# Performance work log

Measured on AMD Instinct MI355X. Metric: run time of the kernel, lower is better.

The kernel has to match this reference:

```python
import jax, jax.numpy as jnp
import numpy as np

ALPHA = 0.2  # leaky relu slope
NEG = -9e15


def setup_inputs() -> dict:
    key = jax.random.key(0)
    k1, k2, k3, k4 = jax.random.split(key, 4)
    B, N, Fin, Fout = 16, 2048, 256, 256
    h = jax.random.normal(k1, (B, N, Fin), dtype=jnp.float32)
    adj = jax.random.randint(k2, (B, N, N), 0, 2, dtype=jnp.int32)
    # xavier_uniform with gain 1.414 on [B, Fin, Fout] (fan over last two dims)
    limW = 1.414 * np.sqrt(6.0 / (Fin + Fout))
    W = jax.random.uniform(k3, (B, Fin, Fout), minval=-limW, maxval=limW, dtype=jnp.float32)
    lima = 1.414 * np.sqrt(6.0 / (2 * Fout + 1))
    a = jax.random.uniform(k4, (B, 2 * Fout, 1), minval=-lima, maxval=lima, dtype=jnp.float32)
    return {"h": h, "adj": adj, "W": W, "a": a}


def reference(h, adj, W, a):
    Fout = W.shape[-1]
    Wh = jnp.einsum('bnf,bfo->bno', h, W)                 # [B,N,Fout]
    Wh1 = jnp.einsum('bno,bo->bn', Wh, a[:, :Fout, 0])    # [B,N]
    Wh2 = jnp.einsum('bno,bo->bn', Wh, a[:, Fout:, 0])    # [B,N]
    e = Wh1[:, :, None] + Wh2[:, None, :]                 # [B,N,N]
    e = jnp.where(e > 0, e, ALPHA * e)                    # leaky relu
    att = jnp.where(adj > 0, e, NEG)
    att = jax.nn.softmax(att, axis=1)                     # NOTE: dim=1 as in source
    # dropout: eval mode -> identity
    h_prime = jnp.einsum('bij,bjo->bio', att, Wh)         # [B,N,Fout]
    return jax.nn.elu(h_prime)                            # concat=True
```

## Files before the change

kernel.cpp:

```cpp
#include <hip/hip_runtime.h>
#include <hip/hip_bf16.h>

typedef unsigned short u16;
typedef unsigned long long u64;
typedef __attribute__((ext_vector_type(8))) short bf16x8;
typedef __attribute__((ext_vector_type(4))) float f32x4;

#define NB 16
#define NN 2048
#define FF 256
#define LOG2E 1.4426950408889634f

__device__ __forceinline__ u16 f2bf(float x) {
    union { float f; unsigned u; } v; v.f = x;
    unsigned r = v.u + 0x7fffu + ((v.u >> 16) & 1u);
    return (u16)(r >> 16);
}

#define GLD_LDS(g, l) __builtin_amdgcn_global_load_lds((const __attribute__((address_space(1))) void*)(g), (__attribute__((address_space(3))) void*)(l), 16, 0, 0)

__global__ __launch_bounds__(256) void k_prep_w(const float* __restrict__ W, const float* __restrict__ a,
                                                u16* __restrict__ WT, float* __restrict__ u1, float* __restrict__ u2) {
    int b = blockIdx.y, t = threadIdx.x;
    __shared__ float a1s[FF], a2s[FF];
    a1s[t] = a[b*2*FF + t];
    a2s[t] = a[b*2*FF + FF + t];
    __syncthreads();
    int f = blockIdx.x*64 + (t >> 2);
    int o0 = (t & 3) * 64;
    const float* wrow = W + (size_t)(b*FF + f)*FF + o0;
    u16* wtb = WT + (size_t)b*FF*FF;
    float s1 = 0.f, s2 = 0.f;
#pragma unroll
    for (int c = 0; c < 16; ++c) {
        float4 v = *(const float4*)(wrow + c*4);
        int o = o0 + c*4;
        s1 += v.x*a1s[o] + v.y*a1s[o+1] + v.z*a1s[o+2] + v.w*a1s[o+3];
        s2 += v.x*a2s[o] + v.y*a2s[o+1] + v.z*a2s[o+2] + v.w*a2s[o+3];
        wtb[(size_t)(o+0)*FF + f] = f2bf(v.x);
        wtb[(size_t)(o+1)*FF + f] = f2bf(v.y);
        wtb[(size_t)(o+2)*FF + f] = f2bf(v.z);
        wtb[(size_t)(o+3)*FF + f] = f2bf(v.w);
    }
    s1 += __shfl_xor(s1, 1); s1 += __shfl_xor(s1, 2);
    s2 += __shfl_xor(s2, 1); s2 += __shfl_xor(s2, 2);
    if ((t & 3) == 0) { u1[b*FF + f] = s1; u2[b*FF + f] = s2; }
}

__global__ __launch_bounds__(256) void k_prep_h(const float* __restrict__ h, const float* __restrict__ u1,
                                                const float* __restrict__ u2, u16* __restrict__ hbf,
                                                float* __restrict__ Wh1, float* __restrict__ Wh2) {
    int b = blockIdx.y, t = threadIdx.x;
    __shared__ float u1s[FF], u2s[FF];
    u1s[t] = u1[b*FF + t];
    u2s[t] = u2[b*FF + t];
    __syncthreads();
    int wave = t >> 6, lane = t & 63;
    int i = blockIdx.x*4 + wave;
    size_t rowoff = ((size_t)(b*NN + i))*FF + lane*4;
    float4 v = *(const float4*)(h + rowoff);
    u16 h0 = f2bf(v.x), h1 = f2bf(v.y), h2 = f2bf(v.z), h3 = f2bf(v.w);
    unsigned p0 = (unsigned)h0 | ((unsigned)h1 << 16);
    unsigned p1 = (unsigned)h2 | ((unsigned)h3 << 16);
    uint2 pk; pk.x = p0; pk.y = p1;
    *(uint2*)(hbf + rowoff) = pk;
    int o = lane*4;
    float s1 = v.x*u1s[o] + v.y*u1s[o+1] + v.z*u1s[o+2] + v.w*u1s[o+3];
    float s2 = v.x*u2s[o] + v.y*u2s[o+1] + v.z*u2s[o+2] + v.w*u2s[o+3];
#pragma unroll
    for (int off = 32; off > 0; off >>= 1) { s1 += __shfl_xor(s1, off); s2 += __shfl_xor(s2, off); }
    if (lane == 0) { Wh1[b*NN + i] = s1*LOG2E; Wh2[b*NN + i] = s2*LOG2E; }
}

__global__ __launch_bounds__(256) void k_gemm1(const u16* __restrict__ WT, const u16* __restrict__ hbf,
                                               u16* __restrict__ WhT) {
    int b = blockIdx.z;
    int o0 = blockIdx.y * 64;
    int i0 = blockIdx.x * 256;
    int t = threadIdx.x, lane = t & 63, w = t >> 6;
    __shared__ alignas(16) u16 At[64*64];
    __shared__ alignas(16) u16 Btl[256*64];
    const u16* WTb = WT + (size_t)b*FF*FF;
    const u16* hb  = hbf + (size_t)b*NN*FF;

    f32x4 acc[4][4];
#pragma unroll
    for (int x = 0; x < 4; ++x)
#pragma unroll
        for (int y = 0; y < 4; ++y) acc[x][y] = (f32x4)0.f;

    for (int kk = 0; kk < 4; ++kk) {
        int k0 = kk*64;
#pragma unroll
        for (int is = 0; is < 2; ++is) {
            int s = is*256 + t;
            int row = s >> 3, jbp = s & 7;
            int jbl = jbp ^ (row & 7);
            GLD_LDS(WTb + (size_t)(o0+row)*FF + k0 + jbl*8, &At[s*8]);
        }
#pragma unroll
        for (int is = 0; is < 8; ++is) {
            int s = is*256 + t;
            int row = s >> 3, jbp = s & 7;
            int jbl = jbp ^ (row & 7);
            GLD_LDS(hb + (size_t)(i0+row)*FF + k0 + jbl*8, &Btl[s*8]);
        }
        __syncthreads();
#pragma unroll
        for (int kc = 0; kc < 2; ++kc) {
            int jl = kc*4 + (lane >> 4);
            bf16x8 af[4], bfr[4];
#pragma unroll
            for (int mi = 0; mi < 4; ++mi) {
                int r = mi*16 + (lane & 15);
                af[mi] = *(const bf16x8*)&At[r*64 + (jl ^ (r & 7))*8];
            }
#pragma unroll
            for (int ni = 0; ni < 4; ++ni) {
                int r = w*64 + ni*16 + (lane & 15);
                bfr[ni] = *(const bf16x8*)&Btl[r*64 + (jl ^ (r & 7))*8];
            }
#pragma unroll
            for (int mi = 0; mi < 4; ++mi)
#pragma unroll
                for (int ni = 0; ni < 4; ++ni)
                    acc[mi][ni] = __builtin_amdgcn_mfma_f32_16x16x32_bf16(af[mi], bfr[ni], acc[mi][ni], 0, 0, 0);
        }
        __syncthreads();
    }
    u16* Wo = WhT + (size_t)b*FF*NN;
#pragma unroll
    for (int mi = 0; mi < 4; ++mi)
#pragma unroll
        for (int ni = 0; ni < 4; ++ni) {
            int i = i0 + w*64 + ni*16 + (lane & 15);
#pragma unroll
            for (int rr = 0; rr < 4; ++rr) {
                int o = o0 + mi*16 + (lane >> 4)*4 + rr;
                Wo[(size_t)o*NN + i] = f2bf(acc[mi][ni][rr]);
            }
        }
}

__global__ __launch_bounds__(256) void k_colsum(const int* __restrict__ adj, const float* __restrict__ Wh1,
                                                const float* __restrict__ Wh2, float* __restrict__ pS,
                                                u64* __restrict__ packed) {
    int b = blockIdx.z, ic = blockIdx.y, jt = blockIdx.x;
    int t = threadIdx.x, lane = t & 63, wave = t >> 6;
    __shared__ float wh1s[256];
    int ibase = ic*256;
    wh1s[t] = Wh1[b*NN + ibase + t];
    __syncthreads();
    int j = jt*256 + t;
    float wh2j = Wh2[b*NN + j];
    const int* acol = adj + (size_t)b*NN*NN + (size_t)ibase*NN + j;
    u64* prow = packed + ((size_t)(b*NN + ibase))*32 + jt*4 + wave;
    float s = 0.f;
    for (int ii = 0; ii < 256; ii += 8) {
        int v[8];
#pragma unroll
        for (int r = 0; r < 8; ++r) v[r] = acol[(size_t)(ii + r)*NN];
#pragma unroll
        for (int r = 0; r < 8; ++r) {
            bool p = v[r] > 0;
            u64 m = __ballot(p);
            if (lane == 0) prow[(size_t)(ii + r)*32] = m;
            float tt = wh1s[ii + r] + wh2j;
            float lr = fmaxf(tt, 0.2f*tt);
            float e = exp2f(lr);
            s += p ? e : 0.f;
        }
    }
    pS[((size_t)(b*8 + ic))*NN + j] = s;
}

__global__ __launch_bounds__(512, 1) void k_gemm3(const u16* __restrict__ WhT, const u64* __restrict__ packed,
                                                  const float* __restrict__ Wh1, const float* __restrict__ Wh2,
                                                  const float* __restrict__ pS, float* __restrict__ out) {
    int bid = blockIdx.x;
    int nid = (bid & 7)*32 + (bid >> 3);
    int b  = nid >> 4;
    int i0 = (nid & 15) * 128;
    int t = threadIdx.x, lane = t & 63, wave = t >> 6;
    int wm = wave >> 2, wn = wave & 3;
    __shared__ alignas(16) u16 At[2][128*64];
    __shared__ alignas(16) u16 Bt[2][256*64];
    __shared__ float wh2s[NN];
    __shared__ float lss[NN];
    __shared__ float wh1s[128];

#pragma unroll
    for (int c = 0; c < 4; ++c) {
        int idx = c*512 + t;
        wh2s[idx] = Wh2[b*NN + idx];
        float s = 0.f;
#pragma unroll
        for (int cc = 0; cc < 8; ++cc) s += pS[((size_t)(b*8 + cc))*NN + idx];
        lss[idx] = (s > 0.f) ? log2f(s) : __builtin_inff();
    }
    if (t < 128) wh1s[t] = Wh1[b*NN + i0 + t];

    const u16* Wo = WhT + (size_t)b*FF*NN;
    const u16* pk = (const u16*)(packed + ((size_t)b*NN)*32);
    int rA = t >> 2, qA = t & 3;

    f32x4 acc[4][4];
#pragma unroll
    for (int x = 0; x < 4; ++x)
#pragma unroll
        for (int y = 0; y < 4; ++y) acc[x][y] = (f32x4)0.f;

    auto stageB_half = [&](int kk, int bbuf, int hf) {
        int k0 = kk*64;
#pragma unroll
        for (int is = hf*2; is < hf*2 + 2; ++is) {
            int s = is*512 + t;
            int row = s >> 3, jbp = s & 7;
            int jbl = jbp ^ (row & 7);
            GLD_LDS(Wo + (size_t)row*NN + k0 + jbl*8, &Bt[bbuf][s*8]);
        }
    };
    auto genA_half = [&](int kk, int bbuf, int hf) {
        unsigned mask = (unsigned)(pk[(size_t)(i0 + rA)*128 + kk*4 + qA]) >> (hf*8);
        float wh1r = wh1s[rA];
        int jb = kk*64 + qA*16 + hf*8;
        float4 w2a = *(const float4*)&wh2s[jb];
        float4 w2b = *(const float4*)&wh2s[jb+4];
        float4 la  = *(const float4*)&lss[jb];
        float4 lb  = *(const float4*)&lss[jb+4];
        float xs[8] = {w2a.x, w2a.y, w2a.z, w2a.w, w2b.x, w2b.y, w2b.z, w2b.w};
        float lv[8] = {la.x, la.y, la.z, la.w, lb.x, lb.y, lb.z, lb.w};
        union { u16 u[8]; bf16x8 v; } ob;
#pragma unroll
        for (int e = 0; e < 8; ++e) {
            float tt = wh1r + xs[e];
            float lr = fmaxf(tt, 0.2f*tt);
            float pe = exp2f(lr - lv[e]);
            ob.u[e] = ((mask >> e) & 1) ? f2bf(pe) : (u16)0;
        }
        *(bf16x8*)&At[bbuf][rA*64 + (((qA*2 + hf) ^ (rA & 7))*8)] = ob.v;
    };
    auto rdA = [&](int bbuf, int mi, int kc) -> bf16x8 {
        int r = wm*64 + mi*16 + (lane & 15);
        int jl = kc*4 + (lane >> 4);
        return *(const bf16x8*)&At[bbuf][r*64 + ((jl ^ (r & 7))*8)];
    };
    auto rdB = [&](int bbuf, int ni, int kc) -> bf16x8 {
        int r = wn*64 + ni*16 + (lane & 15);
        int jl = kc*4 + (lane >> 4);
        return *(const bf16x8*)&Bt[bbuf][r*64 + ((jl ^ (r & 7))*8)];
    };

#define MM(mi, ni, af, bf) acc[mi][ni] = __builtin_amdgcn_mfma_f32_16x16x32_bf16(af, bf, acc[mi][ni], 0, 0, 0)

    __syncthreads();
    stageB_half(0, 0, 0); stageB_half(0, 0, 1);
    genA_half(0, 0, 0);  genA_half(0, 0, 1);
    __syncthreads();

    int bb = 0;
    for (int kk = 0; kk < 32; ++kk) {
        int nb = bb ^ 1;
        bool pf = (kk + 1 < 32);
        bf16x8 aR0[2][2], aR1[2][2], bR0[2][2], bR1[2][2];

#pragma unroll
        for (int x = 0; x < 2; ++x)
#pragma unroll
            for (int kc = 0; kc < 2; ++kc) { aR0[x][kc] = rdA(bb, x, kc); bR0[x][kc] = rdB(bb, x, kc); }
        if (pf) stageB_half(kk+1, nb, 0);
        __builtin_amdgcn_s_barrier();
        __builtin_amdgcn_s_setprio(1);
        MM(0,0,aR0[0][0],bR0[0][0]); MM(0,1,aR0[0][0],bR0[1][0]);
        MM(1,0,aR0[1][0],bR0[0][0]); MM(1,1,aR0[1][0],bR0[1][0]);
        MM(0,0,aR0[0][1],bR0[0][1]); MM(0,1,aR0[0][1],bR0[1][1]);
        MM(1,0,aR0[1][1],bR0[0][1]); MM(1,1,aR0[1][1],bR0[1][1]);
        __builtin_amdgcn_s_setprio(0);
        __builtin_amdgcn_s_barrier();

#pragma unroll
        for (int x = 0; x < 2; ++x)
#pragma unroll
            for (int kc = 0; kc < 2; ++kc) bR1[x][kc] = rdB(bb, 2 + x, kc);
        if (pf) stageB_half(kk+1, nb, 1);
        __builtin_amdgcn_s_barrier();
        __builtin_amdgcn_s_setprio(1);
        MM(0,2,aR0[0][0],bR1[0][0]); MM(0,3,aR0[0][0],bR1[1][0]);
        MM(1,2,aR0[1][0],bR1[0][0]); MM(1,3,aR0[1][0],bR1[1][0]);
        MM(0,2,aR0[0][1],bR1[0][1]); MM(0,3,aR0[0][1],bR1[1][1]);
        MM(1,2,aR0[1][1],bR1[0][1]); MM(1,3,aR0[1][1],bR1[1][1]);
        __builtin_amdgcn_s_setprio(0);
        __builtin_amdgcn_s_barrier();

#pragma unroll
        for (int x = 0; x < 2; ++x)
#pragma unroll
            for (int kc = 0; kc < 2; ++kc) aR1[x][kc] = rdA(bb, 2 + x, kc);
        if (pf) genA_half(kk+1, nb, 0);
        __builtin_amdgcn_s_barrier();
        __builtin_amdgcn_s_setprio(1);
        MM(2,0,aR1[0][0],bR0[0][0]); MM(2,1,aR1[0][0],bR0[1][0]);
        MM(3,0,aR1[1][0],bR0[0][0]); MM(3,1,aR1[1][0],bR0[1][0]);
        MM(2,0,aR1[0][1],bR0[0][1]); MM(2,1,aR1[0][1],bR0[1][1]);
        MM(3,0,aR1[1][1],bR0[0][1]); MM(3,1,aR1[1][1],bR0[1][1]);
        __builtin_amdgcn_s_setprio(0);
        __builtin_amdgcn_s_barrier();

        if (pf) genA_half(kk+1, nb, 1);
        __builtin_amdgcn_s_setprio(1);
        MM(2,2,aR1[0][0],bR1[0][0]); MM(2,3,aR1[0][0],bR1[1][0]);
        MM(3,2,aR1[1][0],bR1[0][0]); MM(3,3,aR1[1][0],bR1[1][0]);
        MM(2,2,aR1[0][1],bR1[0][1]); MM(2,3,aR1[0][1],bR1[1][1]);
        MM(3,2,aR1[1][1],bR1[0][1]); MM(3,3,aR1[1][1],bR1[1][1]);
        __builtin_amdgcn_s_setprio(0);
        __syncthreads();
        bb = nb;
    }
#undef MM

    float* ob2 = out + ((size_t)b*NN)*FF;
#pragma unroll
    for (int mi = 0; mi < 4; ++mi)
#pragma unroll
        for (int ni = 0; ni < 4; ++ni) {
            int o = wn*64 + ni*16 + (lane & 15);
#pragma unroll
            for (int rr = 0; rr < 4; ++rr) {
                int i = i0 + wm*64 + mi*16 + (lane >> 4)*4 + rr;
                float x = acc[mi][ni][rr];
                float y = (x > 0.f) ? x : (exp2f(x*LOG2E) - 1.f);
                ob2[(size_t)i*FF + o] = y;
            }
        }
}

extern "C" void kernel_launch(void* const* d_in, const int* in_sizes, int n_in,
                              void* d_out, int out_size, void* d_ws, size_t ws_size,
                              hipStream_t stream) {
    const float* h   = (const float*)d_in[0];
    const int*   adj = (const int*)d_in[1];
    const float* W   = (const float*)d_in[2];
    const float* a   = (const float*)d_in[3];
    float* out = (float*)d_out;

    char* w = (char*)d_ws;
    const size_t MB = 1u << 20;
    u16* WT  = (u16*)(w + 0);
    u16* hbf = (u16*)(w + 2*MB);
    u16* WhT = (u16*)(w + 18*MB);
    u64* packed = (u64*)(w + 34*MB);
    float* pS  = (float*)(w + 42*MB);
    float* Wh1 = (float*)(w + 43*MB);
    float* Wh2 = (float*)(w + 43*MB + 131072);
    float* u1  = (float*)(w + 43*MB + 3*131072);
    float* u2  = (float*)(w + 43*MB + 3*131072 + 16384);

    k_prep_w<<<dim3(4, 16), 256, 0, stream>>>(W, a, WT, u1, u2);
    k_prep_h<<<dim3(512, 16), 256, 0, stream>>>(h, u1, u2, hbf, Wh1, Wh2);
    k_gemm1<<<dim3(8, 4, 16), 256, 0, stream>>>(WT, hbf, WhT);
    k_colsum<<<dim3(8, 8, 16), 256, 0, stream>>>(adj, Wh1, Wh2, pS, packed);
    k_gemm3<<<dim3(256, 1), 512, 0, stream>>>(WhT, packed, Wh1, Wh2, pS, out);
}
```

Measured before the change: 174.7 us.

## Fuse h conversion into first GEMM, remap packed mask layout, triple-buffer attention GEMM

Merges the h-to-bf16 conversion and Wh1/Wh2 row dots into the Wh GEMM kernel, so the bf16 copy of h no longer goes through global memory. That kernel now computes all 256 output features per block, with 512 threads and 128 rows. The column-sum kernel remaps its j indices so each row's adjacency bitmask is laid out contiguously. The final GEMM now preloads 64-bit mask words, triple-buffers the B tiles and uses a single barrier per step with explicit waitcnt. This trades extra LDS use and a fragile hand-written waitcnt schedule for fewer kernels, less memory traffic and less synchronisation.

```diff
diff --git a/kernel.cpp b/kernel.cpp
--- a/kernel.cpp
+++ b/kernel.cpp
@@ -47,63 +47,60 @@
     if ((t & 3) == 0) { u1[b*FF + f] = s1; u2[b*FF + f] = s2; }
 }
 
-__global__ __launch_bounds__(256) void k_prep_h(const float* __restrict__ h, const float* __restrict__ u1,
-                                                const float* __restrict__ u2, u16* __restrict__ hbf,
-                                                float* __restrict__ Wh1, float* __restrict__ Wh2) {
-    int b = blockIdx.y, t = threadIdx.x;
+__global__ __launch_bounds__(512) void k_wh(const float* __restrict__ h, const u16* __restrict__ WT,
+                                            const float* __restrict__ u1, const float* __restrict__ u2,
+                                            u16* __restrict__ WhT, float* __restrict__ Wh1, float* __restrict__ Wh2) {
+    int bid = blockIdx.x;
+    int nid = (bid & 7)*32 + (bid >> 3);
+    int b  = nid >> 4;
+    int i0 = (nid & 15) * 128;
+    int t = threadIdx.x, lane = t & 63, wave = t >> 6;
+    int wm = wave >> 1, wn = wave & 1;
+    __shared__ alignas(16) u16 At[256*64];
+    __shared__ alignas(16) u16 Bt[128*64];
     __shared__ float u1s[FF], u2s[FF];
-    u1s[t] = u1[b*FF + t];
-    u2s[t] = u2[b*FF + t];
+    if (t < 256) { u1s[t] = u1[b*FF + t]; u2s[t] = u2[b*FF + t]; }
+
+    const u16*   WTb = WT + (size_t)b*FF*FF;
+    const float* hb  = h + ((size_t)b*NN + i0)*FF;
+    int r = t >> 2, q = t & 3, kq = q*16;
+
+    f32x4 acc[4][4];
+#pragma unroll
+    for (int x = 0; x < 4; ++x)
+#pragma unroll
+        for (int y = 0; y < 4; ++y) acc[x][y] = (f32x4)0.f;
+    float s1 = 0.f, s2 = 0.f;
     __syncthreads();
-    int wave = t >> 6, lane = t & 63;
-    int i = blockIdx.x*4 + wave;
-    size_t rowoff = ((size_t)(b*NN + i))*FF + lane*4;
-    float4 v = *(const float4*)(h + rowoff);
-    u16 h0 = f2bf(v.x), h1 = f2bf(v.y), h2 = f2bf(v.z), h3 = f2bf(v.w);
-    unsigned p0 = (unsigned)h0 | ((unsigned)h1 << 16);
-    unsigned p1 = (unsigned)h2 | ((unsigned)h3 << 16);
-    uint2 pk; pk.x = p0; pk.y = p1;
-    *(uint2*)(hbf + rowoff) = pk;
-    int o = lane*4;
-    float s1 = v.x*u1s[o] + v.y*u1s[o+1] + v.z*u1s[o+2] + v.w*u1s[o+3];
-    float s2 = v.x*u2s[o] + v.y*u2s[o+1] + v.z*u2s[o+2] + v.w*u2s[o+3];
-#pragma unroll
-    for (int off = 32; off > 0; off >>= 1) { s1 += __shfl_xor(s1, off); s2 += __shfl_xor(s2, off); }
-    if (lane == 0) { Wh1[b*NN + i] = s1*LOG2E; Wh2[b*NN + i] = s2*LOG2E; }
-}
-
-__global__ __launch_bounds__(256) void k_gemm1(const u16* __restrict__ WT, const u16* __restrict__ hbf,
-                                               u16* __restrict__ WhT) {
-    int b = blockIdx.z;
-    int o0 = blockIdx.y * 64;
-    int i0 = blockIdx.x * 256;
-    int t = threadIdx.x, lane = t & 63, w = t >> 6;
-    __shared__ alignas(16) u16 At[64*64];
-    __shared__ alignas(16) u16 Btl[256*64];
-    const u16* WTb = WT + (size_t)b*FF*FF;
-    const u16* hb  = hbf + (size_t)b*NN*FF;
-
-    f32x4 acc[4][4];
-#pragma unroll
-    for (int x = 0; x < 4; ++x)
-#pragma unroll
-        for (int y = 0; y < 4; ++y) acc[x][y] = (f32x4)0.f;
 
     for (int kk = 0; kk < 4; ++kk) {
         int k0 = kk*64;
 #pragma unroll
-        for (int is = 0; is < 2; ++is) {
-            int s = is*256 + t;
+        for (int is = 0; is < 4; ++is) {
+            int s = is*512 + t;
             int row = s >> 3, jbp = s & 7;
             int jbl = jbp ^ (row & 7);
-            GLD_LDS(WTb + (size_t)(o0+row)*FF + k0 + jbl*8, &At[s*8]);
-        }
-#pragma unroll
-        for (int is = 0; is < 8; ++is) {
-            int s = is*256 + t;
-            int row = s >> 3, jbp = s & 7;
-            int jbl = jbp ^ (row & 7);
-            GLD_LDS(hb + (size_t)(i0+row)*FF + k0 + jbl*8, &Btl[s*8]);
+            GLD_LDS(WTb + (size_t)row*FF + k0 + jbl*8, &At[s*8]);
+        }
+        {
+            const float* hp = hb + (size_t)r*FF + k0 + kq;
+            float4 f0 = *(const float4*)(hp + 0);
+            float4 f1 = *(const float4*)(hp + 4);
+            float4 f2 = *(const float4*)(hp + 8);
+            float4 f3 = *(const float4*)(hp + 12);
+            float fv[16] = {f0.x,f0.y,f0.z,f0.w, f1.x,f1.y,f1.z,f1.w,
+                            f2.x,f2.y,f2.z,f2.w, f3.x,f3.y,f3.z,f3.w};
+            union { u16 u[16]; bf16x8 v[2]; } cv;
+#pragma unroll
+            for (int e = 0; e < 16; ++e) {
+                int kidx = k0 + kq + e;
+                s1 += fv[e]*u1s[kidx];
+                s2 += fv[e]*u2s[kidx];
+                cv.u[e] = f2bf(fv[e]);
+            }
+            int rx = r & 7;
+            *(bf16x8*)&Bt[r*64 + ((q*2 + 0) ^ rx)*8] = cv.v[0];
+            *(bf16x8*)&Bt[r*64 + ((q*2 + 1) ^ rx)*8] = cv.v[1];
         }
         __syncthreads();
 #pragma unroll
@@ -112,13 +109,13 @@
             bf16x8 af[4], bfr[4];
 #pragma unroll
             for (int mi = 0; mi < 4; ++mi) {
-                int r = mi*16 + (lane & 15);
-                af[mi] = *(const bf16x8*)&At[r*64 + (jl ^ (r & 7))*8];
+                int rr2 = wm*64 + mi*16 + (lane & 15);
+                af[mi] = *(const bf16x8*)&At[rr2*64 + ((jl ^ (rr2 & 7))*8)];
             }
 #pragma unroll
             for (int ni = 0; ni < 4; ++ni) {
-                int r = w*64 + ni*16 + (lane & 15);
-                bfr[ni] = *(const bf16x8*)&Btl[r*64 + (jl ^ (r & 7))*8];
+                int rr2 = wn*64 + ni*16 + (lane & 15);
+                bfr[ni] = *(const bf16x8*)&Bt[rr2*64 + ((jl ^ (rr2 & 7))*8)];
             }
 #pragma unroll
             for (int mi = 0; mi < 4; ++mi)
@@ -128,15 +125,19 @@
         }
         __syncthreads();
     }
+    s1 += __shfl_xor(s1, 1); s1 += __shfl_xor(s1, 2);
+    s2 += __shfl_xor(s2, 1); s2 += __shfl_xor(s2, 2);
+    if (q == 0) { Wh1[b*NN + i0 + r] = s1*LOG2E; Wh2[b*NN + i0 + r] = s2*LOG2E; }
+
     u16* Wo = WhT + (size_t)b*FF*NN;
 #pragma unroll
     for (int mi = 0; mi < 4; ++mi)
 #pragma unroll
         for (int ni = 0; ni < 4; ++ni) {
-            int i = i0 + w*64 + ni*16 + (lane & 15);
+            int i = i0 + wn*64 + ni*16 + (lane & 15);
 #pragma unroll
             for (int rr = 0; rr < 4; ++rr) {
-                int o = o0 + mi*16 + (lane >> 4)*4 + rr;
+                int o = wm*64 + mi*16 + (lane >> 4)*4 + rr;
                 Wo[(size_t)o*NN + i] = f2bf(acc[mi][ni][rr]);
             }
         }
@@ -151,21 +152,21 @@
     int ibase = ic*256;
     wh1s[t] = Wh1[b*NN + ibase + t];
     __syncthreads();
-    int j = jt*256 + t;
+    int j = jt*256 + wave*16 + (lane & 15) + (lane >> 4)*64;
     float wh2j = Wh2[b*NN + j];
     const int* acol = adj + (size_t)b*NN*NN + (size_t)ibase*NN + j;
-    u64* prow = packed + ((size_t)(b*NN + ibase))*32 + jt*4 + wave;
+    u64* prow = packed + ((size_t)(b*NN + ibase))*32 + wave*8 + jt;
     float s = 0.f;
     for (int ii = 0; ii < 256; ii += 8) {
         int v[8];
 #pragma unroll
-        for (int r = 0; r < 8; ++r) v[r] = acol[(size_t)(ii + r)*NN];
-#pragma unroll
-        for (int r = 0; r < 8; ++r) {
-            bool p = v[r] > 0;
+        for (int rr = 0; rr < 8; ++rr) v[rr] = acol[(size_t)(ii + rr)*NN];
+#pragma unroll
+        for (int rr = 0; rr < 8; ++rr) {
+            bool p = v[rr] > 0;
             u64 m = __ballot(p);
-            if (lane == 0) prow[(size_t)(ii + r)*32] = m;
-            float tt = wh1s[ii + r] + wh2j;
+            if (lane == 0) prow[(size_t)(ii + rr)*32] = m;
+            float tt = wh1s[ii + rr] + wh2j;
             float lr = fmaxf(tt, 0.2f*tt);
             float e = exp2f(lr);
             s += p ? e : 0.f;
@@ -184,10 +185,16 @@
     int t = threadIdx.x, lane = t & 63, wave = t >> 6;
     int wm = wave >> 2, wn = wave & 3;
     __shared__ alignas(16) u16 At[2][128*64];
-    __shared__ alignas(16) u16 Bt[2][256*64];
+    __shared__ alignas(16) u16 Bt[3][256*64];
     __shared__ float wh2s[NN];
     __shared__ float lss[NN];
     __shared__ float wh1s[128];
+
+    const u16* Wo = WhT + (size_t)b*FF*NN;
+    int rA = t >> 2, qA = t & 3;
+    const u64* pkrow = packed + ((size_t)b*NN + i0 + rA)*32 + qA*8;
+    u64 mcur = pkrow[0];
+    u64 mnext = pkrow[1];
 
 #pragma unroll
     for (int c = 0; c < 4; ++c) {
@@ -200,121 +207,108 @@
     }
     if (t < 128) wh1s[t] = Wh1[b*NN + i0 + t];
 
-    const u16* Wo = WhT + (size_t)b*FF*NN;
-    const u16* pk = (const u16*)(packed + ((size_t)b*NN)*32);
-    int rA = t >> 2, qA = t & 3;
-
     f32x4 acc[4][4];
 #pragma unroll
     for (int x = 0; x < 4; ++x)
 #pragma unroll
         for (int y = 0; y < 4; ++y) acc[x][y] = (f32x4)0.f;
 
-    auto stageB_half = [&](int kk, int bbuf, int hf) {
+    auto stageB = [&](int kk, int bbuf) {
         int k0 = kk*64;
 #pragma unroll
-        for (int is = hf*2; is < hf*2 + 2; ++is) {
+        for (int is = 0; is < 4; ++is) {
             int s = is*512 + t;
             int row = s >> 3, jbp = s & 7;
             int jbl = jbp ^ (row & 7);
             GLD_LDS(Wo + (size_t)row*NN + k0 + jbl*8, &Bt[bbuf][s*8]);
         }
     };
-    auto genA_half = [&](int kk, int bbuf, int hf) {
-        unsigned mask = (unsigned)(pk[(size_t)(i0 + rA)*128 + kk*4 + qA]) >> (hf*8);
+    auto genA = [&](int g, int abuf, unsigned mask16) {
         float wh1r = wh1s[rA];
-        int jb = kk*64 + qA*16 + hf*8;
-        float4 w2a = *(const float4*)&wh2s[jb];
-        float4 w2b = *(const float4*)&wh2s[jb+4];
-        float4 la  = *(const float4*)&lss[jb];
-        float4 lb  = *(const float4*)&lss[jb+4];
-        float xs[8] = {w2a.x, w2a.y, w2a.z, w2a.w, w2b.x, w2b.y, w2b.z, w2b.w};
-        float lv[8] = {la.x, la.y, la.z, la.w, lb.x, lb.y, lb.z, lb.w};
-        union { u16 u[8]; bf16x8 v; } ob;
-#pragma unroll
-        for (int e = 0; e < 8; ++e) {
-            float tt = wh1r + xs[e];
-            float lr = fmaxf(tt, 0.2f*tt);
-            float pe = exp2f(lr - lv[e]);
-            ob.u[e] = ((mask >> e) & 1) ? f2bf(pe) : (u16)0;
-        }
-        *(bf16x8*)&At[bbuf][rA*64 + (((qA*2 + hf) ^ (rA & 7))*8)] = ob.v;
+        int rx = rA & 7;
+#pragma unroll
+        for (int hf = 0; hf < 2; ++hf) {
+            unsigned mask = (mask16 >> (hf*8)) & 0xffu;
+            int jb = g*64 + qA*16 + hf*8;
+            float4 w2a = *(const float4*)&wh2s[jb];
+            float4 w2b = *(const float4*)&wh2s[jb+4];
+            float4 la  = *(const float4*)&lss[jb];
+            float4 lb  = *(const float4*)&lss[jb+4];
+            float xs[8] = {w2a.x, w2a.y, w2a.z, w2a.w, w2b.x, w2b.y, w2b.z, w2b.w};
+            float lv[8] = {la.x, la.y, la.z, la.w, lb.x, lb.y, lb.z, lb.w};
+            union { u16 u[8]; bf16x8 v; } ob;
+#pragma unroll
+            for (int e = 0; e < 8; ++e) {
+                float tt = wh1r + xs[e];
+                float lr = fmaxf(tt, 0.2f*tt);
+                float pe = exp2f(lr - lv[e]);
+                ob.u[e] = ((mask >> e) & 1) ? f2bf(pe) : (u16)0;
+            }
+            *(bf16x8*)&At[abuf][rA*64 + (((qA*2 + hf) ^ rx)*8)] = ob.v;
+        }
     };
-    auto rdA = [&](int bbuf, int mi, int kc) -> bf16x8 {
-        int r = wm*64 + mi*16 + (lane & 15);
-        int jl = kc*4 + (lane >> 4);
-        return *(const bf16x8*)&At[bbuf][r*64 + ((jl ^ (r & 7))*8)];
-    };
-    auto rdB = [&](int bbuf, int ni, int kc) -> bf16x8 {
-        int r = wn*64 + ni*16 + (lane & 15);
-        int jl = kc*4 + (lane >> 4);
-        return *(const bf16x8*)&Bt[bbuf][r*64 + ((jl ^ (r & 7))*8)];
-    };
 
 #define MM(mi, ni, af, bf) acc[mi][ni] = __builtin_amdgcn_mfma_f32_16x16x32_bf16(af, bf, acc[mi][ni], 0, 0, 0)
 
     __syncthreads();
-    stageB_half(0, 0, 0); stageB_half(0, 0, 1);
-    genA_half(0, 0, 0);  genA_half(0, 0, 1);
-    __syncthreads();
-
-    int bb = 0;
+    stageB(0, 0);
+    stageB(1, 1);
+    genA(0, 0, (unsigned)(mcur & 0xffffu));
+    asm volatile("s_waitcnt vmcnt(4) lgkmcnt(0)" ::: "memory");
+    __builtin_amdgcn_s_barrier();
+
+    int ibr = 0, ibs = 2;
     for (int kk = 0; kk < 32; ++kk) {
-        int nb = bb ^ 1;
-        bool pf = (kk + 1 < 32);
-        bf16x8 aR0[2][2], aR1[2][2], bR0[2][2], bR1[2][2];
-
-#pragma unroll
-        for (int x = 0; x < 2; ++x)
-#pragma unroll
-            for (int kc = 0; kc < 2; ++kc) { aR0[x][kc] = rdA(bb, x, kc); bR0[x][kc] = rdB(bb, x, kc); }
-        if (pf) stageB_half(kk+1, nb, 0);
+        if (kk + 2 < 32) stageB(kk + 2, ibs);
+        int g = kk + 1;
+        if (g < 32) {
+            if ((g & 3) == 0) {
+                mcur = mnext;
+                if (g + 4 < 32) mnext = pkrow[(g + 4) >> 2];
+            }
+            unsigned mask16 = (unsigned)((mcur >> ((g & 3)*16)) & 0xffffu);
+            genA(g, g & 1, mask16);
+        }
+        int ra = kk & 1;
+#pragma unroll
+        for (int kc = 0; kc < 2; ++kc) {
+            int jl = kc*4 + (lane >> 4);
+            bf16x8 af[2], bfr[4];
+#pragma unroll
+            for (int mi = 0; mi < 2; ++mi) {
+                int rr2 = wm*64 + mi*16 + (lane & 15);
+                af[mi] = *(const bf16x8*)&At[ra][rr2*64 + ((jl ^ (rr2 & 7))*8)];
+            }
+#pragma unroll
+            for (int ni = 0; ni < 4; ++ni) {
+                int rr2 = wn*64 + ni*16 + (lane & 15);
+                bfr[ni] = *(const bf16x8*)&Bt[ibr][rr2*64 + ((jl ^ (rr2 & 7))*8)];
+            }
+            __builtin_amdgcn_s_setprio(1);
+            MM(0,0,af[0],bfr[0]); MM(0,1,af[0],bfr[1]); MM(0,2,af[0],bfr[2]); MM(0,3,af[0],bfr[3]);
+            MM(1,0,af[1],bfr[0]); MM(1,1,af[1],bfr[1]); MM(1,2,af[1],bfr[2]); MM(1,3,af[1],bfr[3]);
+            __builtin_amdgcn_s_setprio(0);
+            bf16x8 af2[2];
+#pragma unroll
+            for (int mi = 0; mi < 2; ++mi) {
+                int rr2 = 128 + wm*64 + mi*16 + (lane & 15) - 64;
+                (void)rr2;
+            }
+#pragma unroll
+            for (int mi = 2; mi < 4; ++mi) {
+                int rr2 = wm*64 + mi*16 + (lane & 15);
+                af2[mi-2] = *(const bf16x8*)&At[ra][rr2*64 + ((jl ^ (rr2 & 7))*8)];
+            }
+            __builtin_amdgcn_s_setprio(1);
+            MM(2,0,af2[0],bfr[0]); MM(2,1,af2[0],bfr[1]); MM(2,2,af2[0],bfr[2]); MM(2,3,af2[0],bfr[3]);
+            MM(3,0,af2[1],bfr[0]); MM(3,1,af2[1],bfr[1]); MM(3,2,af2[1],bfr[2]); MM(3,3,af2[1],bfr[3]);
+            __builtin_amdgcn_s_setprio(0);
+        }
+        if (kk < 30) asm volatile("s_waitcnt vmcnt(4) lgkmcnt(0)" ::: "memory");
+        else         asm volatile("s_waitcnt vmcnt(0) lgkmcnt(0)" ::: "memory");
         __builtin_amdgcn_s_barrier();
-        __builtin_amdgcn_s_setprio(1);
-        MM(0,0,aR0[0][0],bR0[0][0]); MM(0,1,aR0[0][0],bR0[1][0]);
-        MM(1,0,aR0[1][0],bR0[0][0]); MM(1,1,aR0[1][0],bR0[1][0]);
-        MM(0,0,aR0[0][1],bR0[0][1]); MM(0,1,aR0[0][1],bR0[1][1]);
-        MM(1,0,aR0[1][1],bR0[0][1]); MM(1,1,aR0[1][1],bR0[1][1]);
-        __builtin_amdgcn_s_setprio(0);
-        __builtin_amdgcn_s_barrier();
-
-#pragma unroll
-        for (int x = 0; x < 2; ++x)
-#pragma unroll
-            for (int kc = 0; kc < 2; ++kc) bR1[x][kc] = rdB(bb, 2 + x, kc);
-        if (pf) stageB_half(kk+1, nb, 1);
-        __builtin_amdgcn_s_barrier();
-        __builtin_amdgcn_s_setprio(1);
-        MM(0,2,aR0[0][0],bR1[0][0]); MM(0,3,aR0[0][0],bR1[1][0]);
-        MM(1,2,aR0[1][0],bR1[0][0]); MM(1,3,aR0[1][0],bR1[1][0]);
-        MM(0,2,aR0[0][1],bR1[0][1]); MM(0,3,aR0[0][1],bR1[1][1]);
-        MM(1,2,aR0[1][1],bR1[0][1]); MM(1,3,aR0[1][1],bR1[1][1]);
-        __builtin_amdgcn_s_setprio(0);
-        __builtin_amdgcn_s_barrier();
-
-#pragma unroll
-        for (int x = 0; x < 2; ++x)
-#pragma unroll
-            for (int kc = 0; kc < 2; ++kc) aR1[x][kc] = rdA(bb, 2 + x, kc);
-        if (pf) genA_half(kk+1, nb, 0);
-        __builtin_amdgcn_s_barrier();
-        __builtin_amdgcn_s_setprio(1);
-        MM(2,0,aR1[0][0],bR0[0][0]); MM(2,1,aR1[0][0],bR0[1][0]);
-        MM(3,0,aR1[1][0],bR0[0][0]); MM(3,1,aR1[1][0],bR0[1][0]);
-        MM(2,0,aR1[0][1],bR0[0][1]); MM(2,1,aR1[0][1],bR0[1][1]);
-        MM(3,0,aR1[1][1],bR0[0][1]); MM(3,1,aR1[1][1],bR0[1][1]);
-        __builtin_amdgcn_s_setprio(0);
-        __builtin_amdgcn_s_barrier();
-
-        if (pf) genA_half(kk+1, nb, 1);
-        __builtin_amdgcn_s_setprio(1);
-        MM(2,2,aR1[0][0],bR1[0][0]); MM(2,3,aR1[0][0],bR1[1][0]);
-        MM(3,2,aR1[1][0],bR1[0][0]); MM(3,3,aR1[1][0],bR1[1][0]);
-        MM(2,2,aR1[0][1],bR1[0][1]); MM(2,3,aR1[0][1],bR1[1][1]);
-        MM(3,2,aR1[1][1],bR1[0][1]); MM(3,3,aR1[1][1],bR1[1][1]);
-        __builtin_amdgcn_s_setprio(0);
-        __syncthreads();
-        bb = nb;
+        ibr = (ibr + 1 == 3) ? 0 : ibr + 1;
+        ibs = (ibs + 1 == 3) ? 0 : ibs + 1;
     }
 #undef MM
 
@@ -346,18 +340,16 @@
     char* w = (char*)d_ws;
     const size_t MB = 1u << 20;
     u16* WT  = (u16*)(w + 0);
-    u16* hbf = (u16*)(w + 2*MB);
-    u16* WhT = (u16*)(w + 18*MB);
-    u64* packed = (u64*)(w + 34*MB);
-    float* pS  = (float*)(w + 42*MB);
-    float* Wh1 = (float*)(w + 43*MB);
-    float* Wh2 = (float*)(w + 43*MB + 131072);
-    float* u1  = (float*)(w + 43*MB + 3*131072);
-    float* u2  = (float*)(w + 43*MB + 3*131072 + 16384);
+    u16* WhT = (u16*)(w + 2*MB);
+    u64* packed = (u64*)(w + 18*MB);
+    float* pS  = (float*)(w + 26*MB);
+    float* Wh1 = (float*)(w + 27*MB);
+    float* Wh2 = (float*)(w + 27*MB + 131072);
+    float* u1  = (float*)(w + 27*MB + 2*131072);
+    float* u2  = (float*)(w + 27*MB + 2*131072 + 16384);
 
     k_prep_w<<<dim3(4, 16), 256, 0, stream>>>(W, a, WT, u1, u2);
-    k_prep_h<<<dim3(512, 16), 256, 0, stream>>>(h, u1, u2, hbf, Wh1, Wh2);
-    k_gemm1<<<dim3(8, 4, 16), 256, 0, stream>>>(WT, hbf, WhT);
+    k_wh<<<dim3(256), 512, 0, stream>>>(h, WT, u1, u2, WhT, Wh1, Wh2);
     k_colsum<<<dim3(8, 8, 16), 256, 0, stream>>>(adj, Wh1, Wh2, pS, packed);
-    k_gemm3<<<dim3(256, 1), 512, 0, stream>>>(WhT, packed, Wh1, Wh2, pS, out);
-}
+    k_gemm3<<<dim3(256), 512, 0, stream>>>(WhT, packed, Wh1, Wh2, pS, out);
+}
```

New measurement: 168.5 us. -3.6%, faster.
